# Performance work log

Hardware: AMD Instinct MI355X
Metric: run time of the kernel (lower is better)

## Reference

```python
import jax, jax.numpy as jnp
import numpy as np
import math

T, B, H, L = 512, 64, 512, 2
STDV = 1.0 / math.sqrt(H)


def setup_inputs() -> dict:
    key = jax.random.key(0)
    ks = jax.random.split(key, 16)
    u = lambda k, shape: jax.random.uniform(k, shape, jnp.float32, -STDV, STDV)
    inp = {
        "x": jax.random.normal(ks[0], (T, B, H), jnp.float32),
        "init_states": jax.random.normal(ks[1], (L, B, H), jnp.float32),
        # stacked per-layer GRU cell parameters (input_size == hidden_size)
        "w_ir": u(ks[2], (L, H, H)), "w_hr": u(ks[3], (L, H, H)),
        "w_iz": u(ks[4], (L, H, H)), "w_hz": u(ks[5], (L, H, H)),
        "w_in": u(ks[6], (L, H, H)), "w_hn": u(ks[7], (L, H, H)),
        "b_ir": u(ks[8], (L, H)), "b_hr": u(ks[9], (L, H)),
        "b_iz": u(ks[10], (L, H)), "b_hz": u(ks[11], (L, H)),
        "b_in": u(ks[12], (L, H)), "b_hn": u(ks[13], (L, H)),
    }
    return inp


def _gru_layer(inputs, h0, w_ir, w_hr, w_iz, w_hz, w_in, w_hn,
               b_ir, b_hr, b_iz, b_hz, b_in, b_hn):
    # inputs: [T, B, H]; h0: [B, H]
    def step(h, xt):
        r = jax.nn.sigmoid(xt @ w_ir + b_ir + h @ w_hr + b_hr)
        z = jax.nn.sigmoid(xt @ w_iz + b_iz + h @ w_hz + b_hz)
        n = jnp.tanh(xt @ w_in + b_in + r * (h @ w_hn + b_hn))
        h_new = (1.0 - z) * n + z * h
        return h_new, h_new
    h_last, hs = jax.lax.scan(step, h0, inputs)
    return hs, h_last  # [T, B, H], [B, H]


def reference(x, init_states, w_ir, w_hr, w_iz, w_hz, w_in, w_hn,
              b_ir, b_hr, b_iz, b_hz, b_in, b_hn):
    num_layers = w_ir.shape[0]
    inputs = x
    finals = []
    for l in range(num_layers):
        inputs, h_last = _gru_layer(
            inputs, init_states[l],
            w_ir[l], w_hr[l], w_iz[l], w_hz[l], w_in[l], w_hn[l],
            b_ir[l], b_hr[l], b_iz[l], b_hz[l], b_in[l], b_hn[l])
        finals.append(h_last)
    # (last-layer outputs over all timesteps [T,B,H], per-layer final hidden [L,B,H])
    return inputs, jnp.stack(finals, axis=0)
```

## Files before the change

### kernel.cpp

```cpp
#include <hip/hip_runtime.h>
#include <math.h>


typedef short bf16x8 __attribute__((ext_vector_type(8)));
typedef float f32x4 __attribute__((ext_vector_type(4)));

__device__ __forceinline__ unsigned short f2bf(float f) {
  unsigned u = __builtin_bit_cast(unsigned, f);
  return (unsigned short)((u + 0x7fff + ((u >> 16) & 1)) >> 16);
}
__device__ __forceinline__ unsigned long long ldq(const unsigned long long* p) {
  return __hip_atomic_load(p, __ATOMIC_RELAXED, __HIP_MEMORY_SCOPE_AGENT);
}
__device__ __forceinline__ void stq(unsigned long long* p,
                                    unsigned long long v) {
  __hip_atomic_store(p, v, __ATOMIC_RELAXED, __HIP_MEMORY_SCOPE_AGENT);
}

__device__ __forceinline__ int hchunk(int k, int b) {
  return ((b >> 4) * 16 + (k >> 5)) * 64 + ((k >> 3) & 3) * 16 + (b & 15);
}

__device__ __forceinline__ void grid_barrier(unsigned* bar, unsigned target) {
  __syncthreads();
  if (threadIdx.x == 0) {
    unsigned leaf = blockIdx.x & 7u;
    unsigned prev = __hip_atomic_fetch_add(bar + leaf * 32, 1u,
                                           __ATOMIC_RELAXED,
                                           __HIP_MEMORY_SCOPE_AGENT);
    bool done = false;
    if ((prev & 15u) == 15u) {
      unsigned p2 = __hip_atomic_fetch_add(bar + 256, 1u, __ATOMIC_RELAXED,
                                           __HIP_MEMORY_SCOPE_AGENT);
      if ((p2 & 7u) == 7u) {
        __hip_atomic_store(bar + 288, target, __ATOMIC_RELAXED,
                           __HIP_MEMORY_SCOPE_AGENT);
        done = true;
      }
    }
    if (!done) {
      while (__hip_atomic_load(bar + 288, __ATOMIC_RELAXED,
                               __HIP_MEMORY_SCOPE_AGENT) < target) {
        __builtin_amdgcn_s_sleep(1);
      }
    }
  }
  __syncthreads();
}

__global__ void gru_prep_h(const float* __restrict__ init,
                           unsigned short* __restrict__ h0buf,
                           unsigned short* __restrict__ h1buf,
                           unsigned* __restrict__ bar) {
  int l = blockIdx.x >> 6;
  int idx = (blockIdx.x & 63) * 512 + threadIdx.x;
  int k = idx >> 6, b = idx & 63;
  unsigned short v = f2bf(init[(size_t)l * 32768 + b * 512 + k]);
  unsigned short* dst = (l == 0) ? h0buf : h1buf;
  dst[hchunk(k, b) * 8 + (k & 7)] = v;
  if (blockIdx.x == 0 && threadIdx.x < 512) bar[threadIdx.x] = 0u;
}

__global__ void gru_xprep(const float* __restrict__ x,
                          unsigned short* __restrict__ xbf) {
  int t = blockIdx.x;
#pragma unroll
  for (int it = 0; it < 8; ++it) {
    int ck = it * 512 + threadIdx.x;
    int b = (ck >> 10) * 16 + (ck & 15);
    int k0 = ((ck >> 6) & 15) * 32 + ((ck >> 4) & 3) * 8;
    const float* src = x + ((size_t)t * 64 + b) * 512 + k0;
    float4 v0 = *(const float4*)(src);
    float4 v1 = *(const float4*)(src + 4);
    unsigned short o[8] = {f2bf(v0.x), f2bf(v0.y), f2bf(v0.z), f2bf(v0.w),
                           f2bf(v1.x), f2bf(v1.y), f2bf(v1.z), f2bf(v1.w)};
    *(uint4*)(xbf + (size_t)t * 32768 + ck * 8) = *(const uint4*)o;
  }
}

__global__ void gru_wimg(const float* __restrict__ Wir,
                         const float* __restrict__ Wiz,
                         const float* __restrict__ Win,
                         const float* __restrict__ Whr,
                         const float* __restrict__ Whz,
                         const float* __restrict__ Whn,
                         unsigned short* __restrict__ wX,
                         unsigned short* __restrict__ wH) {
  int l = blockIdx.x >> 6, blk = blockIdx.x & 63;
  size_t base = ((size_t)l * 64 + blk) * 32 * 512;
  size_t wbase = (size_t)l * 512 * 512;
  for (int idx = threadIdx.x; idx < 16384; idx += 256) {
    int c = idx & 7, k = (idx >> 3) & 511, q = idx >> 12;
    int col = blk * 8 + c;
    int row = c * 4 + q;
    size_t we = wbase + (size_t)k * 512 + col;
    float vx = 0.f, vh = 0.f;
    if (q == 0) { vx = Wir[we]; vh = Whr[we]; }
    else if (q == 1) { vx = Wiz[we]; vh = Whz[we]; }
    else if (q == 2) { vx = Win[we]; }
    else { vh = Whn[we]; }
    wX[base + (size_t)row * 512 + k] = f2bf(vx);
    wH[base + (size_t)row * 512 + k] = f2bf(vh);
  }
}

__global__ __launch_bounds__(512, 2) void gru_recur_fused(
    const unsigned short* __restrict__ xbf,
    const unsigned short* __restrict__ wX,
    const unsigned short* __restrict__ wH,
    const float* __restrict__ bir, const float* __restrict__ bhr,
    const float* __restrict__ biz, const float* __restrict__ bhz,
    const float* __restrict__ bin_, const float* __restrict__ bhn,
    const float* __restrict__ init,
    unsigned short* h0buf, unsigned short* h1buf,
    float* __restrict__ Yout, float* __restrict__ finals, unsigned* bar) {
  __shared__ float ghp[2][32][66];
  __shared__ unsigned short hpack[64 * 8];
  const int tid = threadIdx.x;
  const int lane = tid & 63;
  const int wv = tid >> 6;
  const int Nt = wv & 3, Kh = wv >> 2;
  const int quad = lane >> 4, mm = lane & 15;
  const int role = blockIdx.x >> 6;
  const int blk = blockIdx.x & 63;
  const int cg0 = blk * 8;
  const int c = wv, bb = lane;
  const int cg = cg0 + c;
  const float bR = bir[role * 512 + cg] + bhr[role * 512 + cg];
  const float bZ = biz[role * 512 + cg] + bhz[role * 512 + cg];
  const float bNX = bin_[role * 512 + cg];
  const float bNH = bhn[role * 512 + cg];

  bf16x8 aX0[8], aX1[8], aH0[8], aH1[8];
  {
    const unsigned short* wXb = wX + ((size_t)role * 64 + blk) * 32 * 512;
    const unsigned short* wHb = wH + ((size_t)role * 64 + blk) * 32 * 512;
#pragma unroll
    for (int j = 0; j < 8; ++j) {
      int ko = (Kh * 8 + j) * 32 + quad * 8;
      aX0[j] = *(const bf16x8*)(wXb + (size_t)mm * 512 + ko);
      aX1[j] = *(const bf16x8*)(wXb + (size_t)(16 + mm) * 512 + ko);
      aH0[j] = *(const bf16x8*)(wHb + (size_t)mm * 512 + ko);
      aH1[j] = *(const bf16x8*)(wHb + (size_t)(16 + mm) * 512 + ko);
    }
  }
  float hp = init[(size_t)role * 32768 + bb * 512 + cg];

  for (int s = 0; s <= 512; ++s) {
    const bool active = (role == 0) ? (s < 512) : (s >= 1);
    if (active) {
      const int t = (role == 0) ? s : s - 1;
      const unsigned long long* Xq =
          (const unsigned long long*)((role == 0)
                                          ? (xbf + (size_t)t * 32768)
                                          : (h0buf + (size_t)(s & 1) * 32768));
      const unsigned long long* Hq =
          (const unsigned long long*)((role == 0)
                                          ? (h0buf + (size_t)(s & 1) * 32768)
                                          : (h1buf + (size_t)(t & 1) * 32768));
      unsigned short* Hdst = (role == 0)
                                 ? (h0buf + (size_t)((s + 1) & 1) * 32768)
                                 : (h1buf + (size_t)((t + 1) & 1) * 32768);
      unsigned long long xq[16], hq[16];
#pragma unroll
      for (int j = 0; j < 8; ++j) {
        int base = ((Nt * 16 + Kh * 8 + j) * 64 + lane) << 1;
        if (role == 0) {
          xq[2 * j] = Xq[base];
          xq[2 * j + 1] = Xq[base + 1];
        } else {
          xq[2 * j] = ldq(Xq + base);
          xq[2 * j + 1] = ldq(Xq + base + 1);
        }
        hq[2 * j] = ldq(Hq + base);
        hq[2 * j + 1] = ldq(Hq + base + 1);
      }
      f32x4 acc0 = {0.f, 0.f, 0.f, 0.f}, acc1 = {0.f, 0.f, 0.f, 0.f};
#pragma unroll
      for (int j = 0; j < 8; ++j) {
        union { unsigned long long q[2]; bf16x8 v; } ux, uh;
        ux.q[0] = xq[2 * j]; ux.q[1] = xq[2 * j + 1];
        uh.q[0] = hq[2 * j]; uh.q[1] = hq[2 * j + 1];
        acc0 = __builtin_amdgcn_mfma_f32_16x16x32_bf16(aX0[j], ux.v, acc0, 0, 0, 0);
        acc1 = __builtin_amdgcn_mfma_f32_16x16x32_bf16(aX1[j], ux.v, acc1, 0, 0, 0);
        acc0 = __builtin_amdgcn_mfma_f32_16x16x32_bf16(aH0[j], uh.v, acc0, 0, 0, 0);
        acc1 = __builtin_amdgcn_mfma_f32_16x16x32_bf16(aH1[j], uh.v, acc1, 0, 0, 0);
      }
      {
        float* g = &ghp[Kh][0][0];
        int ncol = Nt * 16 + mm;
#pragma unroll
        for (int r = 0; r < 4; ++r) g[(quad * 4 + r) * 66 + ncol] = acc0[r];
#pragma unroll
        for (int r = 0; r < 4; ++r)
          g[(16 + quad * 4 + r) * 66 + ncol] = acc1[r];
      }
      __syncthreads();
      {
        float gr = ghp[0][c * 4 + 0][bb] + ghp[1][c * 4 + 0][bb];
        float gz = ghp[0][c * 4 + 1][bb] + ghp[1][c * 4 + 1][bb];
        float gnx = ghp[0][c * 4 + 2][bb] + ghp[1][c * 4 + 2][bb];
        float gnh = ghp[0][c * 4 + 3][bb] + ghp[1][c * 4 + 3][bb];
        float r = 1.0f / (1.0f + expf(-(gr + bR)));
        float z = 1.0f / (1.0f + expf(-(gz + bZ)));
        float n = tanhf(gnx + bNX + r * (gnh + bNH));
        float hnew = (1.0f - z) * n + z * hp;
        hp = hnew;
        hpack[bb * 8 + c] = f2bf(hnew);
        if (role == 1) {
          Yout[((size_t)t * 64 + bb) * 512 + cg] = hnew;
          if (t == 511) finals[32768 + bb * 512 + cg] = hnew;
        } else if (t == 511) {
          finals[bb * 512 + cg] = hnew;
        }
      }
      __syncthreads();
      if (tid < 64) {
        int ck = ((tid >> 4) * 16 + (cg0 >> 5)) * 64 + ((cg0 >> 3) & 3) * 16 +
                 (tid & 15);
        const unsigned long long* src =
            (const unsigned long long*)(hpack + tid * 8);
        unsigned long long* dst = (unsigned long long*)(Hdst + (size_t)ck * 8);
        stq(dst, src[0]);
        stq(dst + 1, src[1]);
      }
    }
    grid_barrier(bar, (unsigned)(s + 1));
  }
}

extern "C" void kernel_launch(void* const* d_in, const int* in_sizes, int n_in,
                              void* d_out, int out_size, void* d_ws,
                              size_t ws_size, hipStream_t stream) {
  const float* x = (const float*)d_in[0];
  const float* init = (const float*)d_in[1];
  const float* w_ir = (const float*)d_in[2];
  const float* w_hr = (const float*)d_in[3];
  const float* w_iz = (const float*)d_in[4];
  const float* w_hz = (const float*)d_in[5];
  const float* w_in_ = (const float*)d_in[6];
  const float* w_hn = (const float*)d_in[7];
  const float* b_ir = (const float*)d_in[8];
  const float* b_hr = (const float*)d_in[9];
  const float* b_iz = (const float*)d_in[10];
  const float* b_hz = (const float*)d_in[11];
  const float* b_in_ = (const float*)d_in[12];
  const float* b_hn = (const float*)d_in[13];
  float* out = (float*)d_out;
  float* Y = out;
  float* finals = out + (size_t)512 * 64 * 512;

  unsigned short* xbf = (unsigned short*)d_ws;
  unsigned short* wX = xbf + (size_t)512 * 32768;
  unsigned short* wH = wX + (size_t)2 * 64 * 32 * 512;
  unsigned short* h0buf = wH + (size_t)2 * 64 * 32 * 512;
  unsigned short* h1buf = h0buf + 2 * 32768;
  unsigned* bar = (unsigned*)(h1buf + 2 * 32768);

  gru_prep_h<<<128, 512, 0, stream>>>(init, h0buf, h1buf, bar);
  gru_xprep<<<512, 512, 0, stream>>>(x, xbf);
  gru_wimg<<<128, 256, 0, stream>>>(w_ir, w_iz, w_in_, w_hr, w_hz, w_hn, wX,
                                    wH);
  gru_recur_fused<<<128, 512, 0, stream>>>(
      xbf, wX, wH, b_ir, b_hr, b_iz, b_hz, b_in_, b_hn, init, h0buf, h1buf, Y,
      finals, bar);
}
```

Baseline: 2.587 ms.

## Replace grid barrier with per-block progress flags and quad-buffered layer-0 state

Drops the hierarchical all-block grid barrier after each step. Instead, every block publishes its step counter to a per-block flag, and one wavefront polls all 64 flag pairs until the needed producer steps are done. Layer 0 gets four h buffers so it can run up to two steps ahead of layer 1 without overwriting data still being read. The x loads are issued before the wait and the MFMA accumulators are split into x and h chains. Correctness now rests on relaxed atomics plus the vmcnt wait for ordering, and the wait loop spins with no sleep.

```diff
diff --git a/kernel.cpp b/kernel.cpp
--- a/kernel.cpp
+++ b/kernel.cpp
@@ -16,36 +16,12 @@
                                     unsigned long long v) {
   __hip_atomic_store(p, v, __ATOMIC_RELAXED, __HIP_MEMORY_SCOPE_AGENT);
 }
+__device__ __forceinline__ void stw(unsigned* p, unsigned v) {
+  __hip_atomic_store(p, v, __ATOMIC_RELAXED, __HIP_MEMORY_SCOPE_AGENT);
+}
 
 __device__ __forceinline__ int hchunk(int k, int b) {
   return ((b >> 4) * 16 + (k >> 5)) * 64 + ((k >> 3) & 3) * 16 + (b & 15);
-}
-
-__device__ __forceinline__ void grid_barrier(unsigned* bar, unsigned target) {
-  __syncthreads();
-  if (threadIdx.x == 0) {
-    unsigned leaf = blockIdx.x & 7u;
-    unsigned prev = __hip_atomic_fetch_add(bar + leaf * 32, 1u,
-                                           __ATOMIC_RELAXED,
-                                           __HIP_MEMORY_SCOPE_AGENT);
-    bool done = false;
-    if ((prev & 15u) == 15u) {
-      unsigned p2 = __hip_atomic_fetch_add(bar + 256, 1u, __ATOMIC_RELAXED,
-                                           __HIP_MEMORY_SCOPE_AGENT);
-      if ((p2 & 7u) == 7u) {
-        __hip_atomic_store(bar + 288, target, __ATOMIC_RELAXED,
-                           __HIP_MEMORY_SCOPE_AGENT);
-        done = true;
-      }
-    }
-    if (!done) {
-      while (__hip_atomic_load(bar + 288, __ATOMIC_RELAXED,
-                               __HIP_MEMORY_SCOPE_AGENT) < target) {
-        __builtin_amdgcn_s_sleep(1);
-      }
-    }
-  }
-  __syncthreads();
 }
 
 __global__ void gru_prep_h(const float* __restrict__ init,
@@ -112,7 +88,8 @@
     const float* __restrict__ biz, const float* __restrict__ bhz,
     const float* __restrict__ bin_, const float* __restrict__ bhn,
     const float* __restrict__ init,
-    unsigned short* h0buf, unsigned short* h1buf,
+    unsigned short* h0buf,
+    unsigned short* h1buf,
     float* __restrict__ Yout, float* __restrict__ finals, unsigned* bar) {
   __shared__ float ghp[2][32][66];
   __shared__ unsigned short hpack[64 * 8];
@@ -153,39 +130,58 @@
       const unsigned long long* Xq =
           (const unsigned long long*)((role == 0)
                                           ? (xbf + (size_t)t * 32768)
-                                          : (h0buf + (size_t)(s & 1) * 32768));
+                                          : (h0buf + (size_t)(s & 3) * 32768));
       const unsigned long long* Hq =
           (const unsigned long long*)((role == 0)
-                                          ? (h0buf + (size_t)(s & 1) * 32768)
+                                          ? (h0buf + (size_t)(s & 3) * 32768)
                                           : (h1buf + (size_t)(t & 1) * 32768));
       unsigned short* Hdst = (role == 0)
-                                 ? (h0buf + (size_t)((s + 1) & 1) * 32768)
+                                 ? (h0buf + (size_t)((s + 1) & 3) * 32768)
                                  : (h1buf + (size_t)((t + 1) & 1) * 32768);
       unsigned long long xq[16], hq[16];
+      if (role == 0) {
+#pragma unroll
+        for (int j = 0; j < 8; ++j) {
+          int base = ((Nt * 16 + Kh * 8 + j) * 64 + lane) << 1;
+          xq[2 * j] = Xq[base];
+          xq[2 * j + 1] = Xq[base + 1];
+        }
+      }
+      if (wv == 0) {
+        const int t_lo = s;
+        const int t_hi = (role == 0) ? s - 2 : s;
+        const unsigned long long* fq = (const unsigned long long*)bar + lane;
+        while (true) {
+          unsigned long long pq = ldq(fq);
+          bool ok = ((int)(unsigned)pq >= t_lo) &&
+                    ((int)(unsigned)(pq >> 32) >= t_hi);
+          if (__all(ok)) break;
+        }
+      }
+      __syncthreads();
 #pragma unroll
       for (int j = 0; j < 8; ++j) {
         int base = ((Nt * 16 + Kh * 8 + j) * 64 + lane) << 1;
-        if (role == 0) {
-          xq[2 * j] = Xq[base];
-          xq[2 * j + 1] = Xq[base + 1];
-        } else {
+        if (role == 1) {
           xq[2 * j] = ldq(Xq + base);
           xq[2 * j + 1] = ldq(Xq + base + 1);
         }
         hq[2 * j] = ldq(Hq + base);
         hq[2 * j + 1] = ldq(Hq + base + 1);
       }
-      f32x4 acc0 = {0.f, 0.f, 0.f, 0.f}, acc1 = {0.f, 0.f, 0.f, 0.f};
+      f32x4 a0x = {0.f, 0.f, 0.f, 0.f}, a0h = {0.f, 0.f, 0.f, 0.f};
+      f32x4 a1x = {0.f, 0.f, 0.f, 0.f}, a1h = {0.f, 0.f, 0.f, 0.f};
 #pragma unroll
       for (int j = 0; j < 8; ++j) {
         union { unsigned long long q[2]; bf16x8 v; } ux, uh;
         ux.q[0] = xq[2 * j]; ux.q[1] = xq[2 * j + 1];
         uh.q[0] = hq[2 * j]; uh.q[1] = hq[2 * j + 1];
-        acc0 = __builtin_amdgcn_mfma_f32_16x16x32_bf16(aX0[j], ux.v, acc0, 0, 0, 0);
-        acc1 = __builtin_amdgcn_mfma_f32_16x16x32_bf16(aX1[j], ux.v, acc1, 0, 0, 0);
-        acc0 = __builtin_amdgcn_mfma_f32_16x16x32_bf16(aH0[j], uh.v, acc0, 0, 0, 0);
-        acc1 = __builtin_amdgcn_mfma_f32_16x16x32_bf16(aH1[j], uh.v, acc1, 0, 0, 0);
-      }
+        a0x = __builtin_amdgcn_mfma_f32_16x16x32_bf16(aX0[j], ux.v, a0x, 0, 0, 0);
+        a1x = __builtin_amdgcn_mfma_f32_16x16x32_bf16(aX1[j], ux.v, a1x, 0, 0, 0);
+        a0h = __builtin_amdgcn_mfma_f32_16x16x32_bf16(aH0[j], uh.v, a0h, 0, 0, 0);
+        a1h = __builtin_amdgcn_mfma_f32_16x16x32_bf16(aH1[j], uh.v, a1h, 0, 0, 0);
+      }
+      f32x4 acc0 = a0x + a0h, acc1 = a1x + a1h;
       {
         float* g = &ghp[Kh][0][0];
         int ncol = Nt * 16 + mm;
@@ -215,17 +211,20 @@
         }
       }
       __syncthreads();
-      if (tid < 64) {
-        int ck = ((tid >> 4) * 16 + (cg0 >> 5)) * 64 + ((cg0 >> 3) & 3) * 16 +
-                 (tid & 15);
+      if (wv == 0) {
+        int ck = ((lane >> 4) * 16 + (cg0 >> 5)) * 64 + ((cg0 >> 3) & 3) * 16 +
+                 (lane & 15);
         const unsigned long long* src =
-            (const unsigned long long*)(hpack + tid * 8);
+            (const unsigned long long*)(hpack + lane * 8);
         unsigned long long* dst = (unsigned long long*)(Hdst + (size_t)ck * 8);
         stq(dst, src[0]);
         stq(dst + 1, src[1]);
-      }
+        asm volatile("s_waitcnt vmcnt(0)" ::: "memory");
+        if (lane == 0) stw(bar + 2 * blk + role, (unsigned)(s + 1));
+      }
+    } else {
+      if (tid == 0) stw(bar + 2 * blk + role, (unsigned)(s + 1));
     }
-    grid_barrier(bar, (unsigned)(s + 1));
   }
 }
 
@@ -254,7 +253,7 @@
   unsigned short* wX = xbf + (size_t)512 * 32768;
   unsigned short* wH = wX + (size_t)2 * 64 * 32 * 512;
   unsigned short* h0buf = wH + (size_t)2 * 64 * 32 * 512;
-  unsigned short* h1buf = h0buf + 2 * 32768;
+  unsigned short* h1buf = h0buf + (size_t)4 * 32768;
   unsigned* bar = (unsigned*)(h1buf + 2 * 32768);
 
   gru_prep_h<<<128, 512, 0, stream>>>(init, h0buf, h1buf, bar);
```

Result: slower. 4.072 ms (+57.4%).
